# Optimization experiments

Measured on AMD Instinct MI355X. Metric: run time of the kernel, lower is better.

## Reference

```python
import jax, jax.numpy as jnp
import numpy as np

N_NODES = 100000
SEQ = 16          # spiral length
IN_C = 3
NUM_CLASSES = 12


def _xavier(key, shape):
    fan_out, fan_in = shape
    limit = float(np.sqrt(6.0 / (fan_in + fan_out)))
    return jax.random.uniform(key, shape, jnp.float32, -limit, limit)


def setup_inputs() -> dict:
    key = jax.random.key(0)
    ks = jax.random.split(key, 8)
    x = jax.random.normal(ks[0], (N_NODES, IN_C), jnp.float32)
    indices = jax.random.randint(ks[1], (N_NODES, SEQ), 0, N_NODES, jnp.int64)
    return {
        "x": x,
        "indices": indices,
        "fc0_w": _xavier(ks[2], (16, IN_C)),
        "fc0_b": jnp.zeros((16,), jnp.float32),
        "w1": _xavier(ks[3], (32, 16 * SEQ)),
        "b1": jnp.zeros((32,), jnp.float32),
        "w2": _xavier(ks[4], (64, 32 * SEQ)),
        "b2": jnp.zeros((64,), jnp.float32),
        "w3": _xavier(ks[5], (128, 64 * SEQ)),
        "b3": jnp.zeros((128,), jnp.float32),
        "fc1_w": _xavier(ks[6], (256, 128)),
        "fc1_b": jnp.zeros((256,), jnp.float32),
        "fc2_w": _xavier(ks[7], (NUM_CLASSES, 256)),
        "fc2_b": jnp.zeros((NUM_CLASSES,), jnp.float32),
    }


def _spiral_conv(x, indices, w, b):
    # gather spiral neighborhoods: [N, S, C] -> [N, S*C], then linear
    n = indices.shape[0]
    g = x[indices.reshape(-1)].reshape(n, -1)
    return g @ w.T + b


def reference(x, indices, fc0_w, fc0_b, w1, b1, w2, b2, w3, b3,
              fc1_w, fc1_b, fc2_w, fc2_b):
    h = jax.nn.elu(x @ fc0_w.T + fc0_b)                 # [N, 16]
    h = jax.nn.elu(_spiral_conv(h, indices, w1, b1))    # [N, 32]
    h = jax.nn.elu(_spiral_conv(h, indices, w2, b2))    # [N, 64]
    h = jax.nn.elu(_spiral_conv(h, indices, w3, b3))    # [N, 128]
    h = jax.nn.elu(h @ fc1_w.T + fc1_b)                 # [N, 256]
    # dropout is identity in eval mode
    logits = h @ fc2_w.T + fc2_b                        # [N, num_classes]
    return jax.nn.log_softmax(logits, axis=1)
```

## Files before the change

kernel.cpp:

```cpp
#include <hip/hip_runtime.h>
#include <hip/hip_fp8.h>
#include <math.h>
#include <utility>


typedef __bf16 bf16x8 __attribute__((ext_vector_type(8)));
typedef float f32x16 __attribute__((ext_vector_type(16)));
typedef float f32x2 __attribute__((ext_vector_type(2)));

template <int V> using ic = std::integral_constant<int, V>;

template <typename F, int... Is>
__device__ __forceinline__ void static_for_impl(F&& f, std::integer_sequence<int, Is...>) {
    (f(ic<Is>{}), ...);
}
template <int N_, typename F>
__device__ __forceinline__ void static_for(F&& f) {
    static_for_impl(static_cast<F&&>(f), std::make_integer_sequence<int, N_>{});
}

template <int N_>
__device__ __forceinline__ void wait_vmcnt() {
    static_assert(N_ <= 63, "vmcnt range");
    __builtin_amdgcn_s_waitcnt((N_ & 0xF) | (0x7 << 4) | (0xF << 8) | ((N_ >> 4) << 14));
}

__device__ __forceinline__ void memfence_sched() { __builtin_amdgcn_sched_barrier(0x000F); }

__device__ __forceinline__ float elu_f(float v) { return v > 0.f ? v : expm1f(v); }

__device__ __forceinline__ unsigned char to_fp8(float v) {
    int p = __builtin_amdgcn_cvt_pk_fp8_f32(v, v, 0, false);
    return (unsigned char)p;
}

__device__ __forceinline__ unsigned int pk_bf16(float a, float b) {
    unsigned int r;
    asm("v_cvt_pk_bf16_f32 %0, %1, %2" : "=v"(r) : "v"(a), "v"(b));
    return r;
}

__device__ __forceinline__ bf16x8 dq8(long v) {
    unsigned int lo = (unsigned int)(unsigned long)v;
    unsigned int hi = (unsigned int)((unsigned long)v >> 32);
    f32x2 f0 = __builtin_amdgcn_cvt_pk_f32_fp8((int)lo, false);
    f32x2 f1 = __builtin_amdgcn_cvt_pk_f32_fp8((int)lo, true);
    f32x2 f2 = __builtin_amdgcn_cvt_pk_f32_fp8((int)hi, false);
    f32x2 f3 = __builtin_amdgcn_cvt_pk_f32_fp8((int)hi, true);
    union { unsigned int u[4]; bf16x8 b; } r;
    r.u[0] = pk_bf16(f0[0], f0[1]);
    r.u[1] = pk_bf16(f1[0], f1[1]);
    r.u[2] = pk_bf16(f2[0], f2[1]);
    r.u[3] = pk_bf16(f3[0], f3[1]);
    return r.b;
}

template <int K, int C>
__device__ __forceinline__ void swz_one(const float* __restrict__ src, __bf16* __restrict__ dst, int j)
{
    int col = j / K;
    int k = j & (K - 1);
    int chunk = ((k >> 6) * 8 + ((k & 63) >> 3)) * C + col;
    dst[chunk * 8 + (k & 7)] = (__bf16)src[j];
}

__global__ __launch_bounds__(256) void prep_kernel(const float* __restrict__ w1,
                                                   const float* __restrict__ w2,
                                                   const float* __restrict__ w3,
                                                   const float* __restrict__ f1,
                                                   const float* __restrict__ f2,
                                                   __bf16* __restrict__ d1,
                                                   __bf16* __restrict__ d2,
                                                   __bf16* __restrict__ d3,
                                                   __bf16* __restrict__ df1,
                                                   __bf16* __restrict__ df2p,
                                                   const int* __restrict__ idx,
                                                   int* __restrict__ idxT,
                                                   const float* __restrict__ x,
                                                   const float* __restrict__ fc0_w,
                                                   const float* __restrict__ fc0_b,
                                                   __bf16* __restrict__ h0,
                                                   int N)
{
    int b = blockIdx.x;
    if (b < 832) {
        int i = b * 256 + threadIdx.x;
        if (i < 8192)        swz_one<256, 32>(w1, d1, i);
        else if (i < 40960)  swz_one<512, 64>(w2, d2, i - 8192);
        else if (i < 172032) swz_one<1024, 128>(w3, d3, i - 40960);
        else if (i < 204800) swz_one<128, 256>(f1, df1, i - 172032);
        else {
            int d = i - 204800;
            int e = d & 7;
            int chunkIdx = d >> 3;
            int col = chunkIdx & 31;
            int q = chunkIdx >> 5;
            int k = (q >> 3) * 64 + (q & 7) * 8 + e;
            df2p[d] = (col < 12) ? (__bf16)f2[col * 256 + k] : (__bf16)0.f;
        }
    } else if (b < 7082) {
        int i = (b - 832) * 256 + threadIdx.x;
        if (i < N * 16) {
            int n = i >> 4, s = i & 15;
            idxT[s * N + n] = idx[i];
        }
    } else {
        int n = (b - 7082) * 256 + threadIdx.x;
        if (n < N) {
            float x0 = x[n * 3 + 0], x1 = x[n * 3 + 1], x2 = x[n * 3 + 2];
            __bf16 ob[16];
#pragma unroll
            for (int j = 0; j < 16; ++j)
                ob[j] = (__bf16)elu_f(fc0_w[j * 3 + 0] * x0 + fc0_w[j * 3 + 1] * x1
                                      + fc0_w[j * 3 + 2] * x2 + fc0_b[j]);
            int4* dst = (int4*)&h0[(size_t)n * 16];
            dst[0] = *(int4*)&ob[0];
            dst[1] = *(int4*)&ob[8];
        }
    }
}

template <int CIN, int S, int COUT_B, int COUT_TOT, int TILE_M, int RW, int CW,
          bool GATHER, bool OUTF8, int MINW, int NN>
__global__ __launch_bounds__(256, MINW) void mfma_layer(const __bf16* __restrict__ hin,
                                                        const int* __restrict__ idxT,
                                                        const __bf16* __restrict__ Wsw,
                                                        const float* __restrict__ bias,
                                                        void* __restrict__ hout)
{
    constexpr int K = CIN * S;
    constexpr int NSTEP = K / 64;
    static_assert(K % 64 == 0, "K%64");
    constexpr int WM = TILE_M / RW;
    constexpr int WN = COUT_B / CW;
    constexpr int MT = WM / 32;
    constexpr int NT = WN / 32;
    constexpr int IPS = GATHER ? (64 / CIN) : 1;
    constexpr int D = WM / 8;
    constexpr int Bn = NT * 4;
    constexpr int I = GATHER ? D : 0;
    constexpr int NBUFS = 3;
    static_assert(RW * CW == 4, "4 waves");
    static_assert(WM == 32 || WM == 64, "1-2 row subtiles per wave");

    constexpr int AB = 4 * NBUFS * WM * 128;
    constexpr int CB = OUTF8 ? TILE_M * (COUT_B + 16) : TILE_M * (COUT_B + 8) * 2;
    constexpr int SH = AB > CB ? AB : CB;
    __shared__ __align__(16) char smem[SH];

    const int tid = threadIdx.x;
    const int lane = tid & 63;
    const int w = tid >> 6;
    const int wr = w / CW;
    const int wc = w % CW;
    const int ml = lane & 31;
    const int kh = lane >> 5;
    const int m0 = blockIdx.x * TILE_M;
    const int col0 = blockIdx.y * COUT_B;
    const int rbase = m0 + wr * WM;

    char* const Aw = smem + w * (NBUFS * WM * 128);

    int ioff[GATHER ? D : 1];
    int koff[GATHER ? D : 1];
    int gmr[GATHER ? 1 : D];
    int coff[GATHER ? 1 : D];
#pragma unroll
    for (int i = 0; i < D; ++i) {
        int r = i * 8 + (lane >> 3);
        int c = (lane & 7) ^ (r & 7);
        int gm = rbase + r; if (gm >= NN) gm = NN - 1;
        if constexpr (GATHER) {
            ioff[i] = ((c * 8) / CIN) * NN + gm;
            koff[i] = (c * 8) & (CIN - 1);
        } else {
            gmr[i] = gm;
            coff[i] = c * 8;
        }
    }

    bf16x8 bfr[2][NT][4];
    int myIdx[GATHER ? 3 : 1][GATHER ? D : 1];

    const __bf16* wlane = Wsw + ((size_t)(col0 + wc * WN + ml) + (size_t)kh * COUT_TOT) * 8;

    auto loadB = [&](auto sc) {
        constexpr int s = decltype(sc)::value;
        if constexpr (s < NSTEP) {
#pragma unroll
            for (int ni = 0; ni < NT; ++ni)
#pragma unroll
                for (int ks = 0; ks < 4; ++ks)
                    bfr[s & 1][ni][ks] = *(const bf16x8*)(wlane
                        + (size_t)(s * 8 + ks * 2) * COUT_TOT * 8 + ni * 32 * 8);
        }
    };
    auto loadIdxS = [&](auto sc) {
        constexpr int s = decltype(sc)::value;
        if constexpr (GATHER && s < NSTEP) {
#pragma unroll
            for (int i = 0; i < D; ++i)
                myIdx[s % 3][i] = idxT[(s * IPS) * NN + ioff[i]];
        }
    };
    auto issueDMA = [&](auto sc) {
        constexpr int s = decltype(sc)::value;
        if constexpr (s < NSTEP) {
            char* base = Aw + (s % NBUFS) * (WM * 128);
#pragma unroll
            for (int i = 0; i < D; ++i) {
                const __bf16* src;
                if constexpr (GATHER)
                    src = hin + (size_t)myIdx[s % 3][i] * CIN + koff[i];
                else
                    src = hin + (size_t)gmr[i] * K + s * 64 + coff[i];
                __builtin_amdgcn_global_load_lds(
                    (const __attribute__((address_space(1))) void*)src,
                    (__attribute__((address_space(3))) void*)(base + i * 1024),
                    16, 0, 0);
            }
        }
    };

    f32x16 acc[MT][NT];
#pragma unroll
    for (int mi = 0; mi < MT; ++mi)
#pragma unroll
        for (int ni = 0; ni < NT; ++ni) { f32x16 z = {}; acc[mi][ni] = z; }

    loadIdxS(ic<0>{});
    loadIdxS(ic<1>{});
    loadIdxS(ic<2>{});
    memfence_sched();
    loadB(ic<0>{});
    memfence_sched();
    issueDMA(ic<0>{});
    memfence_sched();
    issueDMA(ic<1>{});
    memfence_sched();
    loadIdxS(ic<3>{});
    memfence_sched();

    static_for<NSTEP>([&](auto sc) {
        constexpr int s = decltype(sc)::value;
        constexpr int NW = D * (s + 1 < NSTEP) + I * (s + 3 < NSTEP);
        wait_vmcnt<NW>();
        memfence_sched();

        const char* base = Aw + (s % NBUFS) * (WM * 128);
        bf16x8 afr[MT][4];
#pragma unroll
        for (int mi = 0; mi < MT; ++mi)
#pragma unroll
            for (int ks = 0; ks < 4; ++ks) {
                int cb = ks * 2 + kh;
                afr[mi][ks] = *(const bf16x8*)(base + ((mi * 32 + ml) * 8 + (cb ^ (ml & 7))) * 16);
            }
        memfence_sched();

        loadB(ic<s + 1>{});
        memfence_sched();
        issueDMA(ic<s + 2>{});
        memfence_sched();
        loadIdxS(ic<s + 4>{});
        memfence_sched();

#pragma unroll
        for (int ks = 0; ks < 4; ++ks)
#pragma unroll
            for (int mi = 0; mi < MT; ++mi)
#pragma unroll
                for (int ni = 0; ni < NT; ++ni)
                    acc[mi][ni] = __builtin_amdgcn_mfma_f32_32x32x16_bf16(
                        afr[mi][ks], bfr[s & 1][ni][ks], acc[mi][ni], 0, 0, 0);
    });

    __syncthreads();
    if constexpr (OUTF8) {
        unsigned char* Cs8 = (unsigned char*)smem;
        constexpr int LDC8 = COUT_B + 16;
#pragma unroll
        for (int ni = 0; ni < NT; ++ni) {
            const int col = wc * WN + ni * 32 + ml;
            const float bv = bias[col0 + col];
#pragma unroll
            for (int mi = 0; mi < MT; ++mi) {
#pragma unroll
                for (int r = 0; r < 16; ++r) {
                    int row = wr * WM + mi * 32 + ((r & 3) + 8 * (r >> 2) + 4 * kh);
                    Cs8[row * LDC8 + col] = to_fp8(elu_f(acc[mi][ni][r] + bv));
                }
            }
        }
        __syncthreads();
        constexpr int C16 = COUT_B / 16;
#pragma unroll
        for (int j2 = tid; j2 < TILE_M * C16; j2 += 256) {
            int row = j2 / C16, c16 = j2 % C16;
            int gm = m0 + row;
            if (gm < NN)
                *(int4*)((unsigned char*)hout + (size_t)gm * COUT_TOT + col0 + c16 * 16)
                    = *(int4*)&Cs8[row * LDC8 + c16 * 16];
        }
    } else {
        __bf16* Cs = (__bf16*)smem;
        constexpr int LDC = COUT_B + 8;
#pragma unroll
        for (int ni = 0; ni < NT; ++ni) {
            const int col = wc * WN + ni * 32 + ml;
            const float bv = bias[col0 + col];
#pragma unroll
            for (int mi = 0; mi < MT; ++mi) {
#pragma unroll
                for (int r = 0; r < 16; ++r) {
                    int row = wr * WM + mi * 32 + ((r & 3) + 8 * (r >> 2) + 4 * kh);
                    Cs[row * LDC + col] = (__bf16)elu_f(acc[mi][ni][r] + bv);
                }
            }
        }
        __syncthreads();
        constexpr int C8 = COUT_B / 8;
#pragma unroll
        for (int j2 = tid; j2 < TILE_M * C8; j2 += 256) {
            int row = j2 / C8, c8 = j2 % C8;
            int gm = m0 + row;
            if (gm < NN)
                *(int4*)&((__bf16*)hout)[(size_t)gm * COUT_TOT + col0 + c8 * 8] = *(int4*)&Cs[row * LDC + c8 * 8];
        }
    }
}

__global__ __launch_bounds__(256, 3) void mfma3_mixed(const unsigned char* __restrict__ h2f8,
                                                      const int* __restrict__ idxT,
                                                      const __bf16* __restrict__ Wsw,
                                                      const float* __restrict__ bias,
                                                      __bf16* __restrict__ h3)
{
    constexpr int NN = 100000;
    constexpr int NSTEP = 16;
    constexpr int D = 2;
    constexpr int Bn = 8;
    constexpr int I = 2;
    constexpr int NBUFS = 3;
    __shared__ __align__(16) char smem[24576];

    const int tid = threadIdx.x;
    const int lane = tid & 63;
    const int w = tid >> 6;
    const int wr = w >> 1;
    const int wc = w & 1;
    const int ml = lane & 31;
    const int kh = lane >> 5;
    const int m0 = blockIdx.x * 64;
    const int rbase = m0 + wr * 32;

    char* const Aw = smem + w * (NBUFS * 2048);

    int ioff[D], koff[D];
#pragma unroll
    for (int i = 0; i < D; ++i) {
        int r = i * 16 + (lane >> 2);
        int c = (lane & 3) ^ (r & 3) ^ ((r >> 2) & 3);
        int gm = rbase + r; if (gm >= NN) gm = NN - 1;
        ioff[i] = gm;
        koff[i] = c * 16;
    }

    bf16x8 bfr[2][2][4];
    int myIdx[3][D];

    const __bf16* wlane = Wsw + ((size_t)(wc * 64 + ml) + (size_t)kh * 128) * 8;

    auto loadB = [&](auto sc) {
        constexpr int s = decltype(sc)::value;
        if constexpr (s < NSTEP) {
#pragma unroll
            for (int ni = 0; ni < 2; ++ni)
#pragma unroll
                for (int ks = 0; ks < 4; ++ks)
                    bfr[s & 1][ni][ks] = *(const bf16x8*)(wlane
                        + (size_t)(s * 8 + ks * 2) * 128 * 8 + ni * 32 * 8);
        }
    };
    auto loadIdxS = [&](auto sc) {
        constexpr int s = decltype(sc)::value;
        if constexpr (s < NSTEP) {
#pragma unroll
            for (int i = 0; i < D; ++i)
                myIdx[s % 3][i] = idxT[(size_t)s * NN + ioff[i]];
        }
    };
    auto issueDMA = [&](auto sc) {
        constexpr int s = decltype(sc)::value;
        if constexpr (s < NSTEP) {
            char* base = Aw + (s % NBUFS) * 2048;
#pragma unroll
            for (int i = 0; i < D; ++i) {
                const unsigned char* src = h2f8 + (size_t)myIdx[s % 3][i] * 64 + koff[i];
                __builtin_amdgcn_global_load_lds(
                    (const __attribute__((address_space(1))) void*)src,
                    (__attribute__((address_space(3))) void*)(base + i * 1024),
                    16, 0, 0);
            }
        }
    };

    f32x16 acc[2];
    { f32x16 z = {}; acc[0] = z; acc[1] = z; }

    loadIdxS(ic<0>{});
    loadIdxS(ic<1>{});
    loadIdxS(ic<2>{});
    memfence_sched();
    loadB(ic<0>{});
    memfence_sched();
    issueDMA(ic<0>{});
    memfence_sched();
    issueDMA(ic<1>{});
    memfence_sched();
    loadIdxS(ic<3>{});
    memfence_sched();

    static_for<NSTEP>([&](auto sc) {
        constexpr int s = decltype(sc)::value;
        constexpr int NW = (s == 0)
            ? (D * (1 < NSTEP) + I * (3 < NSTEP))
            : (I * (s + 2 < NSTEP) + Bn + D * (s + 1 < NSTEP) + I * (s + 3 < NSTEP));
        wait_vmcnt<NW>();
        memfence_sched();

        const char* base = Aw + (s % NBUFS) * 2048;
        long a8[4];
#pragma unroll
        for (int ks = 0; ks < 4; ++ks)
            a8[ks] = *(const long*)(base + ml * 64
                + (((ks ^ (ml & 3)) ^ ((ml >> 2) & 3)) << 4) + kh * 8);
        memfence_sched();

        loadB(ic<s + 1>{});
        memfence_sched();
        issueDMA(ic<s + 2>{});
        memfence_sched();
        loadIdxS(ic<s + 4>{});
        memfence_sched();

        bf16x8 afr[4];
#pragma unroll
        for (int ks = 0; ks < 4; ++ks)
            afr[ks] = dq8(a8[ks]);
#pragma unroll
        for (int ks = 0; ks < 4; ++ks)
#pragma unroll
            for (int ni = 0; ni < 2; ++ni)
                acc[ni] = __builtin_amdgcn_mfma_f32_32x32x16_bf16(
                    afr[ks], bfr[s & 1][ni][ks], acc[ni], 0, 0, 0);
    });

    __syncthreads();
    __bf16* Cs = (__bf16*)smem;
#pragma unroll
    for (int ni = 0; ni < 2; ++ni) {
        const int col = wc * 64 + ni * 32 + ml;
        const float bv = bias[col];
#pragma unroll
        for (int r = 0; r < 16; ++r) {
            int row = wr * 32 + ((r & 3) + 8 * (r >> 2) + 4 * kh);
            Cs[row * 136 + col] = (__bf16)elu_f(acc[ni][r] + bv);
        }
    }
    __syncthreads();
#pragma unroll
    for (int j2 = tid; j2 < 64 * 16; j2 += 256) {
        int row = j2 >> 4, c8 = j2 & 15;
        int gm = m0 + row;
        if (gm < NN)
            *(int4*)&h3[(size_t)gm * 128 + c8 * 8] = *(int4*)&Cs[row * 136 + c8 * 8];
    }
}

__global__ __launch_bounds__(256, 3) void fc12_kernel(const __bf16* __restrict__ h3,
                                                      const __bf16* __restrict__ Wsw,
                                                      const float* __restrict__ bias1,
                                                      const __bf16* __restrict__ W2p,
                                                      const float* __restrict__ bias2,
                                                      float* __restrict__ out,
                                                      int N)
{
    __shared__ __align__(16) char smem[32 * 264 * 2];
    const int tid = threadIdx.x;
    const int lane = tid & 63;
    const int w = tid >> 6;
    const int ml = lane & 31;
    const int kh = lane >> 5;
    const int m0 = blockIdx.x * 64;

    const __bf16* wlane = Wsw + ((size_t)(w * 64 + ml) + (size_t)kh * 256) * 8;
    bf16x8 bfr[2][2][4];
#pragma unroll
    for (int s = 0; s < 2; ++s)
#pragma unroll
        for (int ni = 0; ni < 2; ++ni)
#pragma unroll
            for (int ks = 0; ks < 4; ++ks)
                bfr[s][ni][ks] = *(const bf16x8*)(wlane
                    + (size_t)(s * 8 + ks * 2) * 256 * 8 + ni * 32 * 8);

    bf16x8 b2f[4];
#pragma unroll
    for (int ks = 0; ks < 4; ++ks)
        b2f[ks] = *(const bf16x8*)&W2p[((w * 8 + ks * 2 + kh) * 32 + ml) * 8];

#pragma unroll
    for (int half = 0; half < 2; ++half) {
        const int mb = m0 + half * 32;
        if (mb >= N) break;
        if (half) __syncthreads();

#pragma unroll
        for (int t = 0; t < 2; ++t) {
            int j = w * 2 + t;
            int lr = j * 4 + (lane >> 4);
            int sc = (lane & 15) ^ (lr & 15);
            const __bf16* src = h3 + (size_t)(mb + lr) * 128 + sc * 8;
            __builtin_amdgcn_global_load_lds(
                (const __attribute__((address_space(1))) void*)src,
                (__attribute__((address_space(3))) void*)(smem + j * 1024),
                16, 0, 0);
        }
        wait_vmcnt<0>();
        __syncthreads();

        f32x16 acc[2];
        { f32x16 z = {}; acc[0] = z; acc[1] = z; }
        const char* Ab = smem;
#pragma unroll
        for (int s = 0; s < 2; ++s) {
            bf16x8 afr[4];
#pragma unroll
            for (int ks = 0; ks < 4; ++ks) {
                int c16 = s * 8 + ks * 2 + kh;
                afr[ks] = *(const bf16x8*)(Ab + ml * 256 + ((c16 ^ (ml & 15)) * 16));
            }
#pragma unroll
            for (int ks = 0; ks < 4; ++ks)
#pragma unroll
                for (int ni = 0; ni < 2; ++ni)
                    acc[ni] = __builtin_amdgcn_mfma_f32_32x32x16_bf16(afr[ks], bfr[s][ni][ks], acc[ni], 0, 0, 0);
        }
        __syncthreads();

        __bf16* Cs = (__bf16*)smem;
#pragma unroll
        for (int ni = 0; ni < 2; ++ni) {
            int col = w * 64 + ni * 32 + ml;
            float bv = bias1[col];
#pragma unroll
            for (int r = 0; r < 16; ++r) {
                int row = (r & 3) + 8 * (r >> 2) + 4 * kh;
                Cs[row * 264 + col] = (__bf16)elu_f(acc[ni][r] + bv);
            }
        }
        __syncthreads();

        bf16x8 a2[4];
#pragma unroll
        for (int ks = 0; ks < 4; ++ks)
            a2[ks] = *(const bf16x8*)&Cs[ml * 264 + w * 64 + ks * 16 + kh * 8];
        f32x16 acc2;
        { f32x16 z = {}; acc2 = z; }
#pragma unroll
        for (int ks = 0; ks < 4; ++ks)
            acc2 = __builtin_amdgcn_mfma_f32_32x32x16_bf16(a2[ks], b2f[ks], acc2, 0, 0, 0);
        __syncthreads();

        float* P = (float*)(smem + w * 4096);
#pragma unroll
        for (int r = 0; r < 16; ++r)
            P[((r & 3) + 8 * (r >> 2) + 4 * kh) * 32 + ml] = acc2[r];
        __syncthreads();

        float4 s4 = make_float4(0.f, 0.f, 0.f, 0.f);
#pragma unroll
        for (int pw = 0; pw < 4; ++pw) {
            float4 v = *(float4*)(smem + pw * 4096 + tid * 16);
            s4.x += v.x; s4.y += v.y; s4.z += v.z; s4.w += v.w;
        }
        __syncthreads();
        *(float4*)(smem + tid * 16) = s4;
        __syncthreads();

        if (tid < 32) {
            const float* L = (float*)smem + tid * 32;
            float logits[12], mx = -1e30f;
#pragma unroll
            for (int o = 0; o < 12; ++o) {
                logits[o] = L[o] + bias2[o];
                mx = fmaxf(mx, logits[o]);
            }
            float s = 0.f;
#pragma unroll
            for (int o = 0; o < 12; ++o) s += expf(logits[o] - mx);
            float lse = mx + logf(s);
            int n = mb + tid;
            float4 o0 = make_float4(logits[0] - lse, logits[1] - lse, logits[2] - lse, logits[3] - lse);
            float4 o1 = make_float4(logits[4] - lse, logits[5] - lse, logits[6] - lse, logits[7] - lse);
            float4 o2 = make_float4(logits[8] - lse, logits[9] - lse, logits[10] - lse, logits[11] - lse);
            *(float4*)&out[(size_t)n * 12 + 0] = o0;
            *(float4*)&out[(size_t)n * 12 + 4] = o1;
            *(float4*)&out[(size_t)n * 12 + 8] = o2;
        }
    }
}

extern "C" void kernel_launch(void* const* d_in, const int* in_sizes, int n_in,
                              void* d_out, int out_size, void* d_ws, size_t ws_size,
                              hipStream_t stream)
{
    const int N = 100000;
    const float* x     = (const float*)d_in[0];
    const int*   idx   = (const int*)  d_in[1];
    const float* fc0_w = (const float*)d_in[2];
    const float* fc0_b = (const float*)d_in[3];
    const float* w1    = (const float*)d_in[4];
    const float* b1    = (const float*)d_in[5];
    const float* w2    = (const float*)d_in[6];
    const float* b2    = (const float*)d_in[7];
    const float* w3    = (const float*)d_in[8];
    const float* b3    = (const float*)d_in[9];
    const float* fc1_w = (const float*)d_in[10];
    const float* fc1_b = (const float*)d_in[11];
    const float* fc2_w = (const float*)d_in[12];
    const float* fc2_b = (const float*)d_in[13];
    float* out = (float*)d_out;

    char* ws = (char*)d_ws;
    const int n_w1 = 32 * 256, n_w2 = 64 * 512, n_w3 = 128 * 1024, n_fc1 = 256 * 128;
    const int n_fc2p = 32 * 256;
    const int n_wb = n_w1 + n_w2 + n_w3 + n_fc1 + n_fc2p;
    __bf16* w1b = (__bf16*)ws;
    __bf16* w2b = w1b + n_w1;
    __bf16* w3b = w2b + n_w2;
    __bf16* f1b = w3b + n_w3;
    __bf16* f2b = f1b + n_fc1;
    size_t off = ((size_t)n_wb * 2 + 4095) & ~(size_t)4095;
    int* idxT = (int*)(ws + off);              off += (size_t)N * 16 * 4;
    __bf16* h0 = (__bf16*)(ws + off);          off += (size_t)N * 16 * 2;
    __bf16* h1 = (__bf16*)(ws + off);          off += (size_t)N * 32 * 2;
    unsigned char* h2f8 = (unsigned char*)(ws + off);  off += (size_t)N * 64;
    __bf16* h3 = (__bf16*)(ws + off);          off += (size_t)N * 128 * 2;

    prep_kernel<<<7473, 256, 0, stream>>>(w1, w2, w3, fc1_w, fc2_w,
                                          w1b, w2b, w3b, f1b, f2b,
                                          idx, idxT, x, fc0_w, fc0_b, h0, N);

    mfma_layer<16, 16, 32, 32, 128, 4, 1, true, false, 3, 100000>
        <<<dim3((N + 127) / 128, 1), 256, 0, stream>>>(h0, idxT, w1b, b1, (void*)h1);
    mfma_layer<32, 16, 64, 64, 128, 4, 1, true, true, 3, 100000>
        <<<dim3((N + 127) / 128, 1), 256, 0, stream>>>(h1, idxT, w2b, b2, (void*)h2f8);
    mfma3_mixed<<<(N + 63) / 64, 256, 0, stream>>>(h2f8, idxT, w3b, b3, h3);
    fc12_kernel<<<(N + 63) / 64, 256, 0, stream>>>(h3, f1b, fc1_b, f2b, fc2_b, out, N);
}
```

Measured before the change: 220.8 us.

## Fuse spiral layer 3 with fc1/fc2/log_softmax into one kernel

Merges the third spiral convolution kernel with the fc1+fc2+log_softmax kernel. The ELU output of layer 3 is written into a swizzled shared-memory tile and consumed directly, instead of round-tripping h3 (N x 128 bf16) through global memory. This removes one kernel launch and a large write-plus-read of the intermediate activation. In exchange, shared memory grows to about 49 KB, launch bounds drop to 2 blocks per CU, and the fc1 weights are now reloaded inside the half loop rather than preloaded.

Measured after the change: 214.8 us. 2.7% less time.

```diff
diff --git a/kernel.cpp b/kernel.cpp
--- a/kernel.cpp
+++ b/kernel.cpp
@@ -330,11 +330,15 @@
     }
 }
 
-__global__ __launch_bounds__(256, 3) void mfma3_mixed(const unsigned char* __restrict__ h2f8,
+__global__ __launch_bounds__(256, 2) void mfma3_fused(const unsigned char* __restrict__ h2f8,
                                                       const int* __restrict__ idxT,
                                                       const __bf16* __restrict__ Wsw,
-                                                      const float* __restrict__ bias,
-                                                      __bf16* __restrict__ h3)
+                                                      const float* __restrict__ bias3,
+                                                      const __bf16* __restrict__ Wf1,
+                                                      const float* __restrict__ bias1,
+                                                      const __bf16* __restrict__ W2p,
+                                                      const float* __restrict__ bias2,
+                                                      float* __restrict__ out)
 {
     constexpr int NN = 100000;
     constexpr int NSTEP = 16;
@@ -342,7 +346,7 @@
     constexpr int Bn = 8;
     constexpr int I = 2;
     constexpr int NBUFS = 3;
-    __shared__ __align__(16) char smem[24576];
+    __shared__ __align__(16) char smem[49664];
 
     const int tid = threadIdx.x;
     const int lane = tid & 63;
@@ -457,99 +461,61 @@
     });
 
     __syncthreads();
-    __bf16* Cs = (__bf16*)smem;
-#pragma unroll
-    for (int ni = 0; ni < 2; ++ni) {
-        const int col = wc * 64 + ni * 32 + ml;
-        const float bv = bias[col];
-#pragma unroll
-        for (int r = 0; r < 16; ++r) {
-            int row = wr * 32 + ((r & 3) + 8 * (r >> 2) + 4 * kh);
-            Cs[row * 136 + col] = (__bf16)elu_f(acc[ni][r] + bv);
+    {
+        char* Ah = smem + wr * 8192;
+#pragma unroll
+        for (int ni = 0; ni < 2; ++ni) {
+            const int col = wc * 64 + ni * 32 + ml;
+            const float bv = bias3[col];
+#pragma unroll
+            for (int r = 0; r < 16; ++r) {
+                int r16 = (r & 3) + 8 * (r >> 2) + 4 * kh;
+                *(__bf16*)(Ah + r16 * 256 + (((col >> 3) ^ (r16 & 15)) << 4) + (col & 7) * 2)
+                    = (__bf16)elu_f(acc[ni][r] + bv);
+            }
         }
     }
     __syncthreads();
-#pragma unroll
-    for (int j2 = tid; j2 < 64 * 16; j2 += 256) {
-        int row = j2 >> 4, c8 = j2 & 15;
-        int gm = m0 + row;
-        if (gm < NN)
-            *(int4*)&h3[(size_t)gm * 128 + c8 * 8] = *(int4*)&Cs[row * 136 + c8 * 8];
-    }
-}
-
-__global__ __launch_bounds__(256, 3) void fc12_kernel(const __bf16* __restrict__ h3,
-                                                      const __bf16* __restrict__ Wsw,
-                                                      const float* __restrict__ bias1,
-                                                      const __bf16* __restrict__ W2p,
-                                                      const float* __restrict__ bias2,
-                                                      float* __restrict__ out,
-                                                      int N)
-{
-    __shared__ __align__(16) char smem[32 * 264 * 2];
-    const int tid = threadIdx.x;
-    const int lane = tid & 63;
-    const int w = tid >> 6;
-    const int ml = lane & 31;
-    const int kh = lane >> 5;
-    const int m0 = blockIdx.x * 64;
-
-    const __bf16* wlane = Wsw + ((size_t)(w * 64 + ml) + (size_t)kh * 256) * 8;
-    bf16x8 bfr[2][2][4];
-#pragma unroll
-    for (int s = 0; s < 2; ++s)
-#pragma unroll
-        for (int ni = 0; ni < 2; ++ni)
-#pragma unroll
-            for (int ks = 0; ks < 4; ++ks)
-                bfr[s][ni][ks] = *(const bf16x8*)(wlane
-                    + (size_t)(s * 8 + ks * 2) * 256 * 8 + ni * 32 * 8);
 
     bf16x8 b2f[4];
 #pragma unroll
     for (int ks = 0; ks < 4; ++ks)
         b2f[ks] = *(const bf16x8*)&W2p[((w * 8 + ks * 2 + kh) * 32 + ml) * 8];
 
+    const __bf16* wlane1 = Wf1 + ((size_t)(w * 64 + ml) + (size_t)kh * 256) * 8;
+    __bf16* Cs2 = (__bf16*)(smem + 16384);
+    char* Pbase = smem + 33280;
+
 #pragma unroll
     for (int half = 0; half < 2; ++half) {
-        const int mb = m0 + half * 32;
-        if (mb >= N) break;
-        if (half) __syncthreads();
-
-#pragma unroll
-        for (int t = 0; t < 2; ++t) {
-            int j = w * 2 + t;
-            int lr = j * 4 + (lane >> 4);
-            int sc = (lane & 15) ^ (lr & 15);
-            const __bf16* src = h3 + (size_t)(mb + lr) * 128 + sc * 8;
-            __builtin_amdgcn_global_load_lds(
-                (const __attribute__((address_space(1))) void*)src,
-                (__attribute__((address_space(3))) void*)(smem + j * 1024),
-                16, 0, 0);
-        }
-        wait_vmcnt<0>();
-        __syncthreads();
-
-        f32x16 acc[2];
-        { f32x16 z = {}; acc[0] = z; acc[1] = z; }
-        const char* Ab = smem;
+        const char* Ab = smem + half * 8192;
+
+        f32x16 acc1[2];
+        { f32x16 z = {}; acc1[0] = z; acc1[1] = z; }
 #pragma unroll
         for (int s = 0; s < 2; ++s) {
-            bf16x8 afr[4];
+            bf16x8 afr1[4];
 #pragma unroll
             for (int ks = 0; ks < 4; ++ks) {
                 int c16 = s * 8 + ks * 2 + kh;
-                afr[ks] = *(const bf16x8*)(Ab + ml * 256 + ((c16 ^ (ml & 15)) * 16));
-            }
+                afr1[ks] = *(const bf16x8*)(Ab + ml * 256 + ((c16 ^ (ml & 15)) * 16));
+            }
+            bf16x8 bfr1[2][4];
+#pragma unroll
+            for (int ni = 0; ni < 2; ++ni)
+#pragma unroll
+                for (int ks = 0; ks < 4; ++ks)
+                    bfr1[ni][ks] = *(const bf16x8*)(wlane1
+                        + (size_t)(s * 8 + ks * 2) * 256 * 8 + ni * 32 * 8);
 #pragma unroll
             for (int ks = 0; ks < 4; ++ks)
 #pragma unroll
                 for (int ni = 0; ni < 2; ++ni)
-                    acc[ni] = __builtin_amdgcn_mfma_f32_32x32x16_bf16(afr[ks], bfr[s][ni][ks], acc[ni], 0, 0, 0);
-        }
-        __syncthreads();
-
-        __bf16* Cs = (__bf16*)smem;
+                    acc1[ni] = __builtin_amdgcn_mfma_f32_32x32x16_bf16(
+                        afr1[ks], bfr1[ni][ks], acc1[ni], 0, 0, 0);
+        }
+        __syncthreads();
+
 #pragma unroll
         for (int ni = 0; ni < 2; ++ni) {
             int col = w * 64 + ni * 32 + ml;
@@ -557,7 +523,7 @@
 #pragma unroll
             for (int r = 0; r < 16; ++r) {
                 int row = (r & 3) + 8 * (r >> 2) + 4 * kh;
-                Cs[row * 264 + col] = (__bf16)elu_f(acc[ni][r] + bv);
+                Cs2[row * 264 + col] = (__bf16)elu_f(acc1[ni][r] + bv);
             }
         }
         __syncthreads();
@@ -565,7 +531,7 @@
         bf16x8 a2[4];
 #pragma unroll
         for (int ks = 0; ks < 4; ++ks)
-            a2[ks] = *(const bf16x8*)&Cs[ml * 264 + w * 64 + ks * 16 + kh * 8];
+            a2[ks] = *(const bf16x8*)&Cs2[ml * 264 + w * 64 + ks * 16 + kh * 8];
         f32x16 acc2;
         { f32x16 z = {}; acc2 = z; }
 #pragma unroll
@@ -573,7 +539,7 @@
             acc2 = __builtin_amdgcn_mfma_f32_32x32x16_bf16(a2[ks], b2f[ks], acc2, 0, 0, 0);
         __syncthreads();
 
-        float* P = (float*)(smem + w * 4096);
+        float* P = (float*)(Pbase + w * 4096);
 #pragma unroll
         for (int r = 0; r < 16; ++r)
             P[((r & 3) + 8 * (r >> 2) + 4 * kh) * 32 + ml] = acc2[r];
@@ -582,32 +548,34 @@
         float4 s4 = make_float4(0.f, 0.f, 0.f, 0.f);
 #pragma unroll
         for (int pw = 0; pw < 4; ++pw) {
-            float4 v = *(float4*)(smem + pw * 4096 + tid * 16);
+            float4 v = *(float4*)(Pbase + pw * 4096 + tid * 16);
             s4.x += v.x; s4.y += v.y; s4.z += v.z; s4.w += v.w;
         }
         __syncthreads();
-        *(float4*)(smem + tid * 16) = s4;
+        *(float4*)(Pbase + tid * 16) = s4;
         __syncthreads();
 
         if (tid < 32) {
-            const float* L = (float*)smem + tid * 32;
-            float logits[12], mx = -1e30f;
-#pragma unroll
-            for (int o = 0; o < 12; ++o) {
-                logits[o] = L[o] + bias2[o];
-                mx = fmaxf(mx, logits[o]);
-            }
-            float s = 0.f;
-#pragma unroll
-            for (int o = 0; o < 12; ++o) s += expf(logits[o] - mx);
-            float lse = mx + logf(s);
-            int n = mb + tid;
-            float4 o0 = make_float4(logits[0] - lse, logits[1] - lse, logits[2] - lse, logits[3] - lse);
-            float4 o1 = make_float4(logits[4] - lse, logits[5] - lse, logits[6] - lse, logits[7] - lse);
-            float4 o2 = make_float4(logits[8] - lse, logits[9] - lse, logits[10] - lse, logits[11] - lse);
-            *(float4*)&out[(size_t)n * 12 + 0] = o0;
-            *(float4*)&out[(size_t)n * 12 + 4] = o1;
-            *(float4*)&out[(size_t)n * 12 + 8] = o2;
+            int n = m0 + half * 32 + tid;
+            if (n < NN) {
+                const float* L = (float*)Pbase + tid * 32;
+                float logits[12], mx = -1e30f;
+#pragma unroll
+                for (int o = 0; o < 12; ++o) {
+                    logits[o] = L[o] + bias2[o];
+                    mx = fmaxf(mx, logits[o]);
+                }
+                float s = 0.f;
+#pragma unroll
+                for (int o = 0; o < 12; ++o) s += expf(logits[o] - mx);
+                float lse = mx + logf(s);
+                float4 o0 = make_float4(logits[0] - lse, logits[1] - lse, logits[2] - lse, logits[3] - lse);
+                float4 o1 = make_float4(logits[4] - lse, logits[5] - lse, logits[6] - lse, logits[7] - lse);
+                float4 o2 = make_float4(logits[8] - lse, logits[9] - lse, logits[10] - lse, logits[11] - lse);
+                *(float4*)&out[(size_t)n * 12 + 0] = o0;
+                *(float4*)&out[(size_t)n * 12 + 4] = o1;
+                *(float4*)&out[(size_t)n * 12 + 8] = o2;
+            }
         }
     }
 }
@@ -647,7 +615,6 @@
     __bf16* h0 = (__bf16*)(ws + off);          off += (size_t)N * 16 * 2;
     __bf16* h1 = (__bf16*)(ws + off);          off += (size_t)N * 32 * 2;
     unsigned char* h2f8 = (unsigned char*)(ws + off);  off += (size_t)N * 64;
-    __bf16* h3 = (__bf16*)(ws + off);          off += (size_t)N * 128 * 2;
 
     prep_kernel<<<7473, 256, 0, stream>>>(w1, w2, w3, fc1_w, fc2_w,
                                           w1b, w2b, w3b, f1b, f2b,
@@ -657,6 +624,6 @@
         <<<dim3((N + 127) / 128, 1), 256, 0, stream>>>(h0, idxT, w1b, b1, (void*)h1);
     mfma_layer<32, 16, 64, 64, 128, 4, 1, true, true, 3, 100000>
         <<<dim3((N + 127) / 128, 1), 256, 0, stream>>>(h1, idxT, w2b, b2, (void*)h2f8);
-    mfma3_mixed<<<(N + 63) / 64, 256, 0, stream>>>(h2f8, idxT, w3b, b3, h3);
-    fc12_kernel<<<(N + 63) / 64, 256, 0, stream>>>(h3, f1b, fc1_b, f2b, fc2_b, out, N);
-}
+    mfma3_fused<<<(N + 63) / 64, 256, 0, stream>>>(h2f8, idxT, w3b, b3,
+                                                   f1b, fc1_b, f2b, fc2_b, out);
+}
```
